# Kernel optimization log

Hardware: AMD Instinct MI355X
Metric: run time of the kernel (lower is better)

The kernel has to match this reference:

```python
import jax, jax.numpy as jnp
import numpy as np

B, S, D, E, K = 4, 2048, 1024, 8, 2
LN_EPS = 1e-5


def setup_inputs() -> dict:
    key = jax.random.key(0)
    ks = jax.random.split(key, 8)
    s = 1.0 / np.sqrt(D)
    return {
        "x": jax.random.normal(ks[0], (B, S, D), dtype=jnp.float32),
        "noise": jax.random.normal(ks[1], (B, S, E), dtype=jnp.float32) * (1.0 / E),
        "W_route": jax.random.uniform(ks[2], (D, E), minval=-s, maxval=s, dtype=jnp.float32),
        "b_route": jax.random.uniform(ks[3], (E,), minval=-s, maxval=s, dtype=jnp.float32),
        "ln_gamma": jnp.ones((E,), dtype=jnp.float32),
        "ln_beta": jnp.zeros((E,), dtype=jnp.float32),
        "W_exp": jax.random.uniform(ks[4], (E, D, D), minval=-s, maxval=s, dtype=jnp.float32),
        "b_exp": jax.random.uniform(ks[5], (E, D), minval=-s, maxval=s, dtype=jnp.float32),
    }


def reference(x, noise, W_route, b_route, ln_gamma, ln_beta, W_exp, b_exp):
    # Routing: Linear(dim, E) -> LayerNorm(E) -> softmax, plus noise
    logits = jnp.einsum("bsd,de->bse", x, W_route) + b_route
    mu = logits.mean(axis=-1, keepdims=True)
    var = logits.var(axis=-1, keepdims=True)
    ln = (logits - mu) / jnp.sqrt(var + LN_EPS) * ln_gamma + ln_beta
    routing = jax.nn.softmax(ln, axis=-1) + noise

    topk_w, topk_i = jax.lax.top_k(routing, K)          # [B,S,K]
    topk_w = jax.nn.softmax(topk_w, axis=-1)

    # Dense all-expert compute (faithful to the naive original)
    expert_out = jnp.einsum("bsd,edf->bsef", x, W_exp) + b_exp  # [B,S,E,D]

    # Gather top-k experts per token and combine
    sel = jnp.take_along_axis(expert_out, topk_i[..., None], axis=2)  # [B,S,K,D]
    return (sel * topk_w[..., None]).sum(axis=2)
```

## Files before the change

### kernel.cpp

```cpp
#include <hip/hip_runtime.h>
#include <hip/hip_bf16.h>


typedef unsigned short u16;
typedef __bf16 bf16x8 __attribute__((ext_vector_type(8)));
typedef float floatx4 __attribute__((ext_vector_type(4)));
typedef unsigned short u16x8 __attribute__((ext_vector_type(8)));

#define NTOK 8192
#define DDIM 1024
#define NEXP 8

__device__ __forceinline__ u16 f2bf(float f) {
    union { float f; unsigned int i; } c; c.f = f;
    unsigned int i = c.i;
    return (u16)((i + 0x7fffu + ((i >> 16) & 1u)) >> 16);
}

__global__ __launch_bounds__(256) void xcast(const float* __restrict__ x,
                                             u16* __restrict__ xb) {
    size_t i = ((size_t)blockIdx.x * 256 + threadIdx.x) * 8;
    float4 a = *(const float4*)(x + i);
    float4 b = *(const float4*)(x + i + 4);
    u16x8 v;
    v[0] = f2bf(a.x); v[1] = f2bf(a.y); v[2] = f2bf(a.z); v[3] = f2bf(a.w);
    v[4] = f2bf(b.x); v[5] = f2bf(b.y); v[6] = f2bf(b.z); v[7] = f2bf(b.w);
    *(u16x8*)(xb + i) = v;
}

__global__ __launch_bounds__(256) void transpose_w(const float* __restrict__ W,
                                                   u16* __restrict__ WT) {
    __shared__ float tileT[64 * 65];
    const int e = blockIdx.z, d0 = blockIdx.y * 64, f0 = blockIdx.x * 64;
    const int t = threadIdx.x;
    const float* src = W + (size_t)e * DDIM * DDIM;
    u16* dst = WT + (size_t)e * DDIM * DDIM;
    const int r = t >> 2, q = t & 3;
    const float* sp = src + (size_t)(d0 + r) * DDIM + f0 + q * 16;
#pragma unroll
    for (int j = 0; j < 4; ++j) {
        float4 v = *(const float4*)(sp + j * 4);
        int c = q * 16 + j * 4;
        tileT[(c + 0) * 65 + r] = v.x;
        tileT[(c + 1) * 65 + r] = v.y;
        tileT[(c + 2) * 65 + r] = v.z;
        tileT[(c + 3) * 65 + r] = v.w;
    }
    __syncthreads();
    const int c2 = t >> 2, dq = (t & 3) * 16;
    u16x8 o0, o1;
#pragma unroll
    for (int i = 0; i < 8; ++i) o0[i] = f2bf(tileT[c2 * 65 + dq + i]);
#pragma unroll
    for (int i = 0; i < 8; ++i) o1[i] = f2bf(tileT[c2 * 65 + dq + 8 + i]);
    u16* dp = dst + (size_t)(f0 + c2) * DDIM + d0 + dq;
    *(u16x8*)dp = o0;
    *(u16x8*)(dp + 8) = o1;
}

__global__ __launch_bounds__(256) void routing_compute(
    const float* __restrict__ x, const float* __restrict__ noise,
    const float* __restrict__ Wr, const float* __restrict__ br,
    const float* __restrict__ gamma, const float* __restrict__ beta,
    int* __restrict__ e01, float2* __restrict__ w01) {
    __shared__ __align__(16) float wrT[NEXP][DDIM];
    const int t = threadIdx.x;
#pragma unroll
    for (int i = 0; i < 8; ++i) {
        int f4 = i * 256 + t;
        int d = f4 >> 1, half = (f4 & 1) * 4;
        float4 v = *(const float4*)&Wr[d * 8 + half];
        wrT[half + 0][d] = v.x; wrT[half + 1][d] = v.y;
        wrT[half + 2][d] = v.z; wrT[half + 3][d] = v.w;
    }
    __syncthreads();

    const int wave = t >> 6, lane = t & 63;
    const int tok = blockIdx.x * 4 + wave;
    const float4* xrow = (const float4*)(x + (size_t)tok * DDIM);
    float acc[8];
#pragma unroll
    for (int e = 0; e < 8; ++e) acc[e] = 0.f;
#pragma unroll
    for (int i = 0; i < 4; ++i) {
        int d4 = i * 64 + lane;
        float4 xv = xrow[d4];
#pragma unroll
        for (int e = 0; e < 8; ++e) {
            float4 wv = *(const float4*)&wrT[e][d4 * 4];
            acc[e] += xv.x * wv.x + xv.y * wv.y + xv.z * wv.z + xv.w * wv.w;
        }
    }
#pragma unroll
    for (int off = 32; off >= 1; off >>= 1) {
#pragma unroll
        for (int e = 0; e < 8; ++e) acc[e] += __shfl_xor(acc[e], off, 64);
    }
    if (lane == 0) {
        float lg[8], mu = 0.f;
#pragma unroll
        for (int e = 0; e < 8; ++e) { lg[e] = acc[e] + br[e]; mu += lg[e]; }
        mu *= 0.125f;
        float var = 0.f;
#pragma unroll
        for (int e = 0; e < 8; ++e) { float d = lg[e] - mu; var += d * d; }
        var *= 0.125f;
        float rstd = rsqrtf(var + 1e-5f);
        float ln[8], mx = -1e30f;
#pragma unroll
        for (int e = 0; e < 8; ++e) {
            ln[e] = (lg[e] - mu) * rstd * gamma[e] + beta[e];
            mx = fmaxf(mx, ln[e]);
        }
        float s = 0.f, p[8];
#pragma unroll
        for (int e = 0; e < 8; ++e) { p[e] = expf(ln[e] - mx); s += p[e]; }
        float inv = 1.f / s, r[8];
#pragma unroll
        for (int e = 0; e < 8; ++e) r[e] = p[e] * inv + noise[(size_t)tok * 8 + e];
        int i0 = 0; float v0 = r[0];
#pragma unroll
        for (int e = 1; e < 8; ++e) if (r[e] > v0) { v0 = r[e]; i0 = e; }
        int i1 = -1; float v1 = -1e30f;
#pragma unroll
        for (int e = 0; e < 8; ++e) if (e != i0 && r[e] > v1) { v1 = r[e]; i1 = e; }
        float w0 = 1.f / (1.f + expf(v1 - v0));
        e01[tok] = i0 | (i1 << 8);
        w01[tok] = make_float2(w0, 1.f - w0);
    }
}

__global__ __launch_bounds__(256) void build_lists(
    const int* __restrict__ e01, const float2* __restrict__ w01,
    int* __restrict__ counts, int* __restrict__ list_tok, float* __restrict__ list_w) {
    const int g = blockIdx.x;
    const int slot = g >> 3, ex = g & 7;
    const int t = threadIdx.x, wave = t >> 6, lane = t & 63;
    __shared__ int wtot[4];
    int base = 0;
    for (int start = 0; start < NTOK; start += 256) {
        int tok = start + t;
        int packed = e01[tok];
        int e = slot ? ((packed >> 8) & 0xff) : (packed & 0xff);
        bool sel = (e == ex);
        unsigned long long m = __ballot(sel);
        int prefix = __popcll(m & ((1ULL << lane) - 1ULL));
        if (lane == 0) wtot[wave] = __popcll(m);
        __syncthreads();
        int wbase = 0;
#pragma unroll
        for (int wv = 0; wv < 4; ++wv) if (wv < wave) wbase += wtot[wv];
        int total = wtot[0] + wtot[1] + wtot[2] + wtot[3];
        if (sel) {
            float2 w2 = w01[tok];
            int pos = base + wbase + prefix;
            list_tok[g * NTOK + pos] = tok;
            list_w[g * NTOK + pos] = slot ? w2.y : w2.x;
        }
        base += total;
        __syncthreads();
    }
    if (t == 0) counts[g] = base;
}

template <int BF16A>
__global__ __launch_bounds__(256) void moe_gemm(
    const float* __restrict__ xf, const u16* __restrict__ xb,
    const u16* __restrict__ WT, const float* __restrict__ bexp,
    const int* __restrict__ counts, const int* __restrict__ list_tok,
    const float* __restrict__ list_w, float* __restrict__ out,
    int grp_base, int accum) {
    const int id = blockIdx.x;
    const int e = id & 7;
    const int n = (id >> 3) & 7;
    const int m = id >> 6;
    const int grp = grp_base + e;
    int cnt = counts[grp];
    cnt = cnt < 0 ? 0 : (cnt > NTOK ? NTOK : cnt);
    const int m0 = m * 128;
    if (m0 >= cnt) return;
    const int n0 = n * 128;

    __shared__ __align__(16) u16 A_s[128 * 64];
    __shared__ __align__(16) u16 B_s[128 * 64];
    __shared__ int tok_s[128];
    __shared__ float w_s[128];
    __shared__ float bias_s[128];

    const int t = threadIdx.x;
    if (t < 128) {
        int r = m0 + t;
        int rr = r < cnt ? r : cnt - 1;
        tok_s[t] = list_tok[grp * NTOK + rr] & (NTOK - 1);
        w_s[t] = (r < cnt) ? list_w[grp * NTOK + rr] : 0.f;
        bias_s[t] = bexp[e * DDIM + n0 + t];
    }
    __syncthreads();

    const int sr = t >> 3;
    const int ch = t & 7;
    const int co = ch * 8;

    size_t arow[4];
    u16 *adst[4], *bdst[4];
#pragma unroll
    for (int s = 0; s < 4; ++s) {
        int row = s * 32 + sr;
        arow[s] = (size_t)tok_s[row] * DDIM + co;
        int cs = ((ch ^ (row & 7)) << 3);
        adst[s] = A_s + row * 64 + cs;
        bdst[s] = B_s + row * 64 + cs;
    }
    const u16* bsrc = WT + ((size_t)e * DDIM + n0 + sr) * DDIM + co;

    const int lane = t & 63, wave = t >> 6;
    const int wm = wave >> 1, wn = wave & 1;
    const int lm = lane & 15, kc = lane >> 4;

    floatx4 acc[4][4];
#pragma unroll
    for (int mi = 0; mi < 4; ++mi)
#pragma unroll
        for (int ni = 0; ni < 4; ++ni) acc[mi][ni] = (floatx4){0.f, 0.f, 0.f, 0.f};

    u16x8 pa[4], pb[4];
    float4 pfa[4][2];
#pragma unroll
    for (int s = 0; s < 4; ++s) {
        if (BF16A) {
            pa[s] = *(const u16x8*)(xb + arow[s]);
        } else {
            pfa[s][0] = *(const float4*)(xf + arow[s]);
            pfa[s][1] = *(const float4*)(xf + arow[s] + 4);
        }
        pb[s] = *(const u16x8*)(bsrc + (size_t)s * 32 * DDIM);
    }

    for (int kk = 0; kk < DDIM; kk += 64) {
        u16x8 wa[4];
#pragma unroll
        for (int s = 0; s < 4; ++s) {
            if (BF16A) {
                wa[s] = pa[s];
            } else {
                wa[s][0] = f2bf(pfa[s][0].x); wa[s][1] = f2bf(pfa[s][0].y);
                wa[s][2] = f2bf(pfa[s][0].z); wa[s][3] = f2bf(pfa[s][0].w);
                wa[s][4] = f2bf(pfa[s][1].x); wa[s][5] = f2bf(pfa[s][1].y);
                wa[s][6] = f2bf(pfa[s][1].z); wa[s][7] = f2bf(pfa[s][1].w);
            }
        }
        __syncthreads();
#pragma unroll
        for (int s = 0; s < 4; ++s) {
            *(u16x8*)adst[s] = wa[s];
            *(u16x8*)bdst[s] = pb[s];
        }
        __syncthreads();
        const int nk = kk + 64;
        if (nk < DDIM) {
#pragma unroll
            for (int s = 0; s < 4; ++s) {
                if (BF16A) {
                    pa[s] = *(const u16x8*)(xb + arow[s] + nk);
                } else {
                    pfa[s][0] = *(const float4*)(xf + arow[s] + nk);
                    pfa[s][1] = *(const float4*)(xf + arow[s] + nk + 4);
                }
                pb[s] = *(const u16x8*)(bsrc + (size_t)s * 32 * DDIM + nk);
            }
        }
#pragma unroll
        for (int ks = 0; ks < 2; ++ks) {
            bf16x8 af[4], bfr[4];
#pragma unroll
            for (int mi = 0; mi < 4; ++mi) {
                int row = wm * 64 + mi * 16 + lm;
                int c = (((ks * 4 + kc) ^ (row & 7)) << 3);
                af[mi] = *(const bf16x8*)&A_s[row * 64 + c];
            }
#pragma unroll
            for (int ni = 0; ni < 4; ++ni) {
                int row = wn * 64 + ni * 16 + lm;
                int c = (((ks * 4 + kc) ^ (row & 7)) << 3);
                bfr[ni] = *(const bf16x8*)&B_s[row * 64 + c];
            }
#pragma unroll
            for (int mi = 0; mi < 4; ++mi)
#pragma unroll
                for (int ni = 0; ni < 4; ++ni)
                    acc[mi][ni] = __builtin_amdgcn_mfma_f32_16x16x32_bf16(
                        af[mi], bfr[ni], acc[mi][ni], 0, 0, 0);
        }
    }

#pragma unroll
    for (int mi = 0; mi < 4; ++mi) {
        int rb = wm * 64 + mi * 16 + (lane >> 4) * 4;
#pragma unroll
        for (int reg = 0; reg < 4; ++reg) {
            int r = rb + reg;
            if (m0 + r < cnt) {
                size_t tok = (size_t)tok_s[r];
                float w = w_s[r];
                float* yrow = out + tok * DDIM + n0;
#pragma unroll
                for (int ni = 0; ni < 4; ++ni) {
                    int col = wn * 64 + ni * 16 + lm;
                    float v = w * (acc[mi][ni][reg] + bias_s[col]);
                    if (accum) v += yrow[col];
                    yrow[col] = v;
                }
            }
        }
    }
}

extern "C" void kernel_launch(void* const* d_in, const int* in_sizes, int n_in,
                              void* d_out, int out_size, void* d_ws, size_t ws_size,
                              hipStream_t stream) {
    const float* x     = (const float*)d_in[0];
    const float* noise = (const float*)d_in[1];
    const float* Wr    = (const float*)d_in[2];
    const float* br    = (const float*)d_in[3];
    const float* gamma = (const float*)d_in[4];
    const float* beta  = (const float*)d_in[5];
    const float* Wexp  = (const float*)d_in[6];
    const float* bexp  = (const float*)d_in[7];
    float* out = (float*)d_out;

    unsigned char* ws = (unsigned char*)d_ws;
    u16* WT       = (u16*)ws;
    int* counts   = (int*)(ws + 16777216);
    int* list_tok = (int*)(ws + 16777472);
    float* list_w = (float*)(ws + 17301760);
    int* e01      = (int*)(ws + 17826048);
    float2* w01   = (float2*)(ws + 17858816);
    u16* xb       = (u16*)(ws + 17924352);
    const size_t need_bf16a = 17924352 + 16777216;

    transpose_w<<<dim3(16, 16, 8), 256, 0, stream>>>(Wexp, WT);
    routing_compute<<<NTOK / 4, 256, 0, stream>>>(x, noise, Wr, br, gamma, beta,
                                                  e01, w01);
    build_lists<<<16, 256, 0, stream>>>(e01, w01, counts, list_tok, list_w);

    if (ws_size >= need_bf16a) {
        xcast<<<NTOK * DDIM / (256 * 8), 256, 0, stream>>>(x, xb);
        moe_gemm<1><<<dim3(4096), 256, 0, stream>>>(
            x, xb, WT, bexp, counts, list_tok, list_w, out, 0, 0);
        moe_gemm<1><<<dim3(4096), 256, 0, stream>>>(
            x, xb, WT, bexp, counts, list_tok, list_w, out, 8, 1);
    } else {
        moe_gemm<0><<<dim3(4096), 256, 0, stream>>>(
            x, xb, WT, bexp, counts, list_tok, list_w, out, 0, 0);
        moe_gemm<0><<<dim3(4096), 256, 0, stream>>>(
            x, xb, WT, bexp, counts, list_tok, list_w, out, 8, 1);
    }
}
```

Before: 239.0 us.

## Fuse bf16 cast into routing and use persistent 128x64 expert GEMM tiles

Removes the separate xcast kernel by writing the bf16 copy of x inside the routing kernel, which already reads every row of x. Restructures the MoE GEMM to a fixed grid of 1024 blocks, each looping over M tiles of its expert's token list with a 128x64 output tile instead of 128x128. The goal is to avoid launching thousands of blocks that exit early and to cut one full pass over x. In exchange the GEMM reloads A tiles twice as often per output element and each block does less MFMA work per LDS stage, and load balance now depends on how tokens are spread across experts.

Result: slower. 248.1 us (+3.8%).

```diff
diff --git a/kernel.cpp b/kernel.cpp
--- a/kernel.cpp
+++ b/kernel.cpp
@@ -6,6 +6,7 @@
 typedef __bf16 bf16x8 __attribute__((ext_vector_type(8)));
 typedef float floatx4 __attribute__((ext_vector_type(4)));
 typedef unsigned short u16x8 __attribute__((ext_vector_type(8)));
+typedef unsigned short u16x4 __attribute__((ext_vector_type(4)));
 
 #define NTOK 8192
 #define DDIM 1024
@@ -15,17 +16,6 @@
     union { float f; unsigned int i; } c; c.f = f;
     unsigned int i = c.i;
     return (u16)((i + 0x7fffu + ((i >> 16) & 1u)) >> 16);
-}
-
-__global__ __launch_bounds__(256) void xcast(const float* __restrict__ x,
-                                             u16* __restrict__ xb) {
-    size_t i = ((size_t)blockIdx.x * 256 + threadIdx.x) * 8;
-    float4 a = *(const float4*)(x + i);
-    float4 b = *(const float4*)(x + i + 4);
-    u16x8 v;
-    v[0] = f2bf(a.x); v[1] = f2bf(a.y); v[2] = f2bf(a.z); v[3] = f2bf(a.w);
-    v[4] = f2bf(b.x); v[5] = f2bf(b.y); v[6] = f2bf(b.z); v[7] = f2bf(b.w);
-    *(u16x8*)(xb + i) = v;
 }
 
 __global__ __launch_bounds__(256) void transpose_w(const float* __restrict__ W,
@@ -58,11 +48,12 @@
     *(u16x8*)(dp + 8) = o1;
 }
 
+template <int WRITE_XB>
 __global__ __launch_bounds__(256) void routing_compute(
     const float* __restrict__ x, const float* __restrict__ noise,
     const float* __restrict__ Wr, const float* __restrict__ br,
     const float* __restrict__ gamma, const float* __restrict__ beta,
-    int* __restrict__ e01, float2* __restrict__ w01) {
+    int* __restrict__ e01, float2* __restrict__ w01, u16* __restrict__ xb) {
     __shared__ __align__(16) float wrT[NEXP][DDIM];
     const int t = threadIdx.x;
 #pragma unroll
@@ -85,6 +76,11 @@
     for (int i = 0; i < 4; ++i) {
         int d4 = i * 64 + lane;
         float4 xv = xrow[d4];
+        if (WRITE_XB) {
+            u16x4 o;
+            o[0] = f2bf(xv.x); o[1] = f2bf(xv.y); o[2] = f2bf(xv.z); o[3] = f2bf(xv.w);
+            *(u16x4*)(xb + (size_t)tok * DDIM + d4 * 4) = o;
+        }
 #pragma unroll
         for (int e = 0; e < 8; ++e) {
             float4 wv = *(const float4*)&wrT[e][d4 * 4];
@@ -172,143 +168,145 @@
     int grp_base, int accum) {
     const int id = blockIdx.x;
     const int e = id & 7;
-    const int n = (id >> 3) & 7;
-    const int m = id >> 6;
+    const int n = (id >> 3) & 15;
+    const int mslot = id >> 7;
     const int grp = grp_base + e;
     int cnt = counts[grp];
     cnt = cnt < 0 ? 0 : (cnt > NTOK ? NTOK : cnt);
-    const int m0 = m * 128;
-    if (m0 >= cnt) return;
-    const int n0 = n * 128;
+    const int n0 = n * 64;
 
     __shared__ __align__(16) u16 A_s[128 * 64];
-    __shared__ __align__(16) u16 B_s[128 * 64];
+    __shared__ __align__(16) u16 B_s[64 * 64];
     __shared__ int tok_s[128];
     __shared__ float w_s[128];
-    __shared__ float bias_s[128];
+    __shared__ float bias_s[64];
 
     const int t = threadIdx.x;
-    if (t < 128) {
-        int r = m0 + t;
-        int rr = r < cnt ? r : cnt - 1;
-        tok_s[t] = list_tok[grp * NTOK + rr] & (NTOK - 1);
-        w_s[t] = (r < cnt) ? list_w[grp * NTOK + rr] : 0.f;
-        bias_s[t] = bexp[e * DDIM + n0 + t];
-    }
-    __syncthreads();
+    if (t < 64) bias_s[t] = bexp[e * DDIM + n0 + t];
 
     const int sr = t >> 3;
     const int ch = t & 7;
     const int co = ch * 8;
-
-    size_t arow[4];
-    u16 *adst[4], *bdst[4];
-#pragma unroll
-    for (int s = 0; s < 4; ++s) {
-        int row = s * 32 + sr;
-        arow[s] = (size_t)tok_s[row] * DDIM + co;
-        int cs = ((ch ^ (row & 7)) << 3);
-        adst[s] = A_s + row * 64 + cs;
-        bdst[s] = B_s + row * 64 + cs;
-    }
+    const int cs = ((ch ^ (sr & 7)) << 3);
     const u16* bsrc = WT + ((size_t)e * DDIM + n0 + sr) * DDIM + co;
 
     const int lane = t & 63, wave = t >> 6;
     const int wm = wave >> 1, wn = wave & 1;
     const int lm = lane & 15, kc = lane >> 4;
 
-    floatx4 acc[4][4];
-#pragma unroll
-    for (int mi = 0; mi < 4; ++mi)
-#pragma unroll
-        for (int ni = 0; ni < 4; ++ni) acc[mi][ni] = (floatx4){0.f, 0.f, 0.f, 0.f};
-
-    u16x8 pa[4], pb[4];
-    float4 pfa[4][2];
-#pragma unroll
-    for (int s = 0; s < 4; ++s) {
-        if (BF16A) {
-            pa[s] = *(const u16x8*)(xb + arow[s]);
-        } else {
-            pfa[s][0] = *(const float4*)(xf + arow[s]);
-            pfa[s][1] = *(const float4*)(xf + arow[s] + 4);
-        }
-        pb[s] = *(const u16x8*)(bsrc + (size_t)s * 32 * DDIM);
-    }
-
-    for (int kk = 0; kk < DDIM; kk += 64) {
-        u16x8 wa[4];
+    for (int m0 = mslot * 128; m0 < cnt; m0 += 1024) {
+        __syncthreads();
+        if (t < 128) {
+            int r = m0 + t;
+            int rr = r < cnt ? r : cnt - 1;
+            tok_s[t] = list_tok[grp * NTOK + rr] & (NTOK - 1);
+            w_s[t] = (r < cnt) ? list_w[grp * NTOK + rr] : 0.f;
+        }
+        __syncthreads();
+
+        size_t arow[4];
+#pragma unroll
+        for (int s = 0; s < 4; ++s)
+            arow[s] = (size_t)tok_s[s * 32 + sr] * DDIM + co;
+
+        floatx4 acc[4][2];
+#pragma unroll
+        for (int mi = 0; mi < 4; ++mi)
+#pragma unroll
+            for (int ni = 0; ni < 2; ++ni) acc[mi][ni] = (floatx4){0.f, 0.f, 0.f, 0.f};
+
+        u16x8 pa[4], pb[2];
+        float4 pfa[4][2];
 #pragma unroll
         for (int s = 0; s < 4; ++s) {
             if (BF16A) {
-                wa[s] = pa[s];
+                pa[s] = *(const u16x8*)(xb + arow[s]);
             } else {
-                wa[s][0] = f2bf(pfa[s][0].x); wa[s][1] = f2bf(pfa[s][0].y);
-                wa[s][2] = f2bf(pfa[s][0].z); wa[s][3] = f2bf(pfa[s][0].w);
-                wa[s][4] = f2bf(pfa[s][1].x); wa[s][5] = f2bf(pfa[s][1].y);
-                wa[s][6] = f2bf(pfa[s][1].z); wa[s][7] = f2bf(pfa[s][1].w);
-            }
-        }
-        __syncthreads();
-#pragma unroll
-        for (int s = 0; s < 4; ++s) {
-            *(u16x8*)adst[s] = wa[s];
-            *(u16x8*)bdst[s] = pb[s];
-        }
-        __syncthreads();
-        const int nk = kk + 64;
-        if (nk < DDIM) {
+                pfa[s][0] = *(const float4*)(xf + arow[s]);
+                pfa[s][1] = *(const float4*)(xf + arow[s] + 4);
+            }
+        }
+#pragma unroll
+        for (int s = 0; s < 2; ++s)
+            pb[s] = *(const u16x8*)(bsrc + (size_t)s * 32 * DDIM);
+
+        for (int kk = 0; kk < DDIM; kk += 64) {
+            u16x8 wa[4];
 #pragma unroll
             for (int s = 0; s < 4; ++s) {
                 if (BF16A) {
-                    pa[s] = *(const u16x8*)(xb + arow[s] + nk);
+                    wa[s] = pa[s];
                 } else {
-                    pfa[s][0] = *(const float4*)(xf + arow[s] + nk);
-                    pfa[s][1] = *(const float4*)(xf + arow[s] + nk + 4);
-                }
-                pb[s] = *(const u16x8*)(bsrc + (size_t)s * 32 * DDIM + nk);
-            }
-        }
-#pragma unroll
-        for (int ks = 0; ks < 2; ++ks) {
-            bf16x8 af[4], bfr[4];
-#pragma unroll
-            for (int mi = 0; mi < 4; ++mi) {
-                int row = wm * 64 + mi * 16 + lm;
-                int c = (((ks * 4 + kc) ^ (row & 7)) << 3);
-                af[mi] = *(const bf16x8*)&A_s[row * 64 + c];
-            }
-#pragma unroll
-            for (int ni = 0; ni < 4; ++ni) {
-                int row = wn * 64 + ni * 16 + lm;
-                int c = (((ks * 4 + kc) ^ (row & 7)) << 3);
-                bfr[ni] = *(const bf16x8*)&B_s[row * 64 + c];
-            }
-#pragma unroll
-            for (int mi = 0; mi < 4; ++mi)
-#pragma unroll
-                for (int ni = 0; ni < 4; ++ni)
-                    acc[mi][ni] = __builtin_amdgcn_mfma_f32_16x16x32_bf16(
-                        af[mi], bfr[ni], acc[mi][ni], 0, 0, 0);
-        }
-    }
-
-#pragma unroll
-    for (int mi = 0; mi < 4; ++mi) {
-        int rb = wm * 64 + mi * 16 + (lane >> 4) * 4;
-#pragma unroll
-        for (int reg = 0; reg < 4; ++reg) {
-            int r = rb + reg;
-            if (m0 + r < cnt) {
-                size_t tok = (size_t)tok_s[r];
-                float w = w_s[r];
-                float* yrow = out + tok * DDIM + n0;
-#pragma unroll
-                for (int ni = 0; ni < 4; ++ni) {
-                    int col = wn * 64 + ni * 16 + lm;
-                    float v = w * (acc[mi][ni][reg] + bias_s[col]);
-                    if (accum) v += yrow[col];
-                    yrow[col] = v;
+                    wa[s][0] = f2bf(pfa[s][0].x); wa[s][1] = f2bf(pfa[s][0].y);
+                    wa[s][2] = f2bf(pfa[s][0].z); wa[s][3] = f2bf(pfa[s][0].w);
+                    wa[s][4] = f2bf(pfa[s][1].x); wa[s][5] = f2bf(pfa[s][1].y);
+                    wa[s][6] = f2bf(pfa[s][1].z); wa[s][7] = f2bf(pfa[s][1].w);
+                }
+            }
+            __syncthreads();
+#pragma unroll
+            for (int s = 0; s < 4; ++s)
+                *(u16x8*)(A_s + (s * 32 + sr) * 64 + cs) = wa[s];
+#pragma unroll
+            for (int s = 0; s < 2; ++s)
+                *(u16x8*)(B_s + (s * 32 + sr) * 64 + cs) = pb[s];
+            __syncthreads();
+            const int nk = kk + 64;
+            if (nk < DDIM) {
+#pragma unroll
+                for (int s = 0; s < 4; ++s) {
+                    if (BF16A) {
+                        pa[s] = *(const u16x8*)(xb + arow[s] + nk);
+                    } else {
+                        pfa[s][0] = *(const float4*)(xf + arow[s] + nk);
+                        pfa[s][1] = *(const float4*)(xf + arow[s] + nk + 4);
+                    }
+                }
+#pragma unroll
+                for (int s = 0; s < 2; ++s)
+                    pb[s] = *(const u16x8*)(bsrc + (size_t)s * 32 * DDIM + nk);
+            }
+#pragma unroll
+            for (int ks = 0; ks < 2; ++ks) {
+                bf16x8 af[4], bfr[2];
+#pragma unroll
+                for (int mi = 0; mi < 4; ++mi) {
+                    int row = wm * 64 + mi * 16 + lm;
+                    int c = (((ks * 4 + kc) ^ (row & 7)) << 3);
+                    af[mi] = *(const bf16x8*)&A_s[row * 64 + c];
+                }
+#pragma unroll
+                for (int ni = 0; ni < 2; ++ni) {
+                    int row = wn * 32 + ni * 16 + lm;
+                    int c = (((ks * 4 + kc) ^ (row & 7)) << 3);
+                    bfr[ni] = *(const bf16x8*)&B_s[row * 64 + c];
+                }
+#pragma unroll
+                for (int mi = 0; mi < 4; ++mi)
+#pragma unroll
+                    for (int ni = 0; ni < 2; ++ni)
+                        acc[mi][ni] = __builtin_amdgcn_mfma_f32_16x16x32_bf16(
+                            af[mi], bfr[ni], acc[mi][ni], 0, 0, 0);
+            }
+        }
+
+#pragma unroll
+        for (int mi = 0; mi < 4; ++mi) {
+            int rb = wm * 64 + mi * 16 + (lane >> 4) * 4;
+#pragma unroll
+            for (int reg = 0; reg < 4; ++reg) {
+                int r = rb + reg;
+                if (m0 + r < cnt) {
+                    size_t tok = (size_t)tok_s[r];
+                    float w = w_s[r];
+                    float* yrow = out + tok * DDIM + n0;
+#pragma unroll
+                    for (int ni = 0; ni < 2; ++ni) {
+                        int col = wn * 32 + ni * 16 + lm;
+                        float v = w * (acc[mi][ni][reg] + bias_s[col]);
+                        if (accum) v += yrow[col];
+                        yrow[col] = v;
+                    }
                 }
             }
         }
@@ -339,20 +337,21 @@
     const size_t need_bf16a = 17924352 + 16777216;
 
     transpose_w<<<dim3(16, 16, 8), 256, 0, stream>>>(Wexp, WT);
-    routing_compute<<<NTOK / 4, 256, 0, stream>>>(x, noise, Wr, br, gamma, beta,
-                                                  e01, w01);
-    build_lists<<<16, 256, 0, stream>>>(e01, w01, counts, list_tok, list_w);
-
     if (ws_size >= need_bf16a) {
-        xcast<<<NTOK * DDIM / (256 * 8), 256, 0, stream>>>(x, xb);
-        moe_gemm<1><<<dim3(4096), 256, 0, stream>>>(
+        routing_compute<1><<<NTOK / 4, 256, 0, stream>>>(x, noise, Wr, br, gamma,
+                                                         beta, e01, w01, xb);
+        build_lists<<<16, 256, 0, stream>>>(e01, w01, counts, list_tok, list_w);
+        moe_gemm<1><<<dim3(1024), 256, 0, stream>>>(
             x, xb, WT, bexp, counts, list_tok, list_w, out, 0, 0);
-        moe_gemm<1><<<dim3(4096), 256, 0, stream>>>(
+        moe_gemm<1><<<dim3(1024), 256, 0, stream>>>(
             x, xb, WT, bexp, counts, list_tok, list_w, out, 8, 1);
     } else {
-        moe_gemm<0><<<dim3(4096), 256, 0, stream>>>(
+        routing_compute<0><<<NTOK / 4, 256, 0, stream>>>(x, noise, Wr, br, gamma,
+                                                         beta, e01, w01, xb);
+        build_lists<<<16, 256, 0, stream>>>(e01, w01, counts, list_tok, list_w);
+        moe_gemm<0><<<dim3(1024), 256, 0, stream>>>(
             x, xb, WT, bexp, counts, list_tok, list_w, out, 0, 0);
-        moe_gemm<0><<<dim3(4096), 256, 0, stream>>>(
+        moe_gemm<0><<<dim3(1024), 256, 0, stream>>>(
             x, xb, WT, bexp, counts, list_tok, list_w, out, 8, 1);
     }
 }
```
